# Kernel optimization log

Measured on AMD Instinct MI355X. Metric: run time of the kernel, lower is better.

## Reference

```python
import jax, jax.numpy as jnp
import numpy as np

B, S, D, H = 2, 2048, 1024, 16
DH = D // H
EPS = 1e-5


def _ln(x, g, b):
    m = jnp.mean(x, axis=-1, keepdims=True)
    v = jnp.mean((x - m) ** 2, axis=-1, keepdims=True)
    return (x - m) * jax.lax.rsqrt(v + EPS) * g + b


def setup_inputs() -> dict:
    key = jax.random.key(0)
    ks = jax.random.split(key, 16)
    w = lambda k, shp: jax.random.normal(k, shp, jnp.float32) * 0.02
    return {
        "x": jax.random.normal(ks[0], (B, S, D), jnp.float32),
        # semantic preprocessor: Linear(D,2D) -> ReLU -> Linear(2D,D), residual + LN
        "pW1": w(ks[1], (D, 2 * D)), "pb1": jnp.zeros((2 * D,), jnp.float32),
        "pW2": w(ks[2], (2 * D, D)), "pb2": jnp.zeros((D,), jnp.float32),
        "gp": jnp.ones((D,), jnp.float32), "bp": jnp.zeros((D,), jnp.float32),
        # multi-head attention projections
        "Wq": w(ks[3], (D, D)), "bq": jnp.zeros((D,), jnp.float32),
        "Wk": w(ks[4], (D, D)), "bk": jnp.zeros((D,), jnp.float32),
        "Wv": w(ks[5], (D, D)), "bv": jnp.zeros((D,), jnp.float32),
        "Wo": w(ks[6], (D, D)), "bo": jnp.zeros((D,), jnp.float32),
        "g1": jnp.ones((D,), jnp.float32), "b1": jnp.zeros((D,), jnp.float32),
        # FFN: Linear(D,4D) -> ReLU -> Linear(4D,D)
        "Wf1": w(ks[7], (D, 4 * D)), "bf1": jnp.zeros((4 * D,), jnp.float32),
        "Wf2": w(ks[8], (4 * D, D)), "bf2": jnp.zeros((D,), jnp.float32),
        "g2": jnp.ones((D,), jnp.float32), "b2": jnp.zeros((D,), jnp.float32),
    }


def reference(x, pW1, pb1, pW2, pb2, gp, bp,
              Wq, bq, Wk, bk, Wv, bv, Wo, bo, g1, b1,
              Wf1, bf1, Wf2, bf2, g2, b2):
    # specialized 'semantic' preprocessor (dropout = identity in eval)
    h = jax.nn.relu(x @ pW1 + pb1) @ pW2 + pb2
    s = _ln(x + h, gp, bp)                       # [B,S,D]
    # naive multi-head attention
    q = (s @ Wq + bq).reshape(B, S, H, DH)
    k = (s @ Wk + bk).reshape(B, S, H, DH)
    v = (s @ Wv + bv).reshape(B, S, H, DH)
    scores = jnp.einsum("bqhd,bkhd->bhqk", q, k) / np.sqrt(DH).astype(np.float32)
    attn = jax.nn.softmax(scores, axis=-1)       # [B,H,S,S]
    ctx = jnp.einsum("bhqk,bkhd->bqhd", attn, v).reshape(B, S, D)
    attn_out = ctx @ Wo + bo
    y = _ln(s + attn_out, g1, b1)
    # FFN (dropouts = identity)
    f = jax.nn.relu(y @ Wf1 + bf1) @ Wf2 + bf2
    return _ln(y + f, g2, b2)
```

## Files before the change

### kernel.cpp

```cpp
#include <hip/hip_runtime.h>
#include <cstdint>
#include <cstddef>

typedef _Float16 f16;
typedef _Float16 f16x8 __attribute__((ext_vector_type(8)));
typedef _Float16 f16x4 __attribute__((ext_vector_type(4)));
typedef float    f32x4 __attribute__((ext_vector_type(4)));
typedef float    f32x16 __attribute__((ext_vector_type(16)));
typedef unsigned int uint2v __attribute__((ext_vector_type(2)));

#define MFMA16(a,b,c) __builtin_amdgcn_mfma_f32_16x16x32_f16(a, b, c, 0, 0, 0)
#define MFMA32(a,b,c) __builtin_amdgcn_mfma_f32_32x32x16_f16(a, b, c, 0, 0, 0)

static __device__ __forceinline__ void gload_lds16(const void* g, void* l) {
  __builtin_amdgcn_global_load_lds(
      (const __attribute__((address_space(1))) unsigned int*)g,
      (__attribute__((address_space(3))) unsigned int*)l, 16, 0, 0);
}

static __device__ __forceinline__ int pkh(float a, float b) {
  auto t = __builtin_amdgcn_cvt_pkrtz(a, b);
  return __builtin_bit_cast(int, t);
}

static __device__ __forceinline__ float ex2(float x) {
  return __builtin_amdgcn_exp2f(x);
}

static __device__ __forceinline__ uint2v pswap(int a, int b) {
  return __builtin_amdgcn_permlane32_swap((unsigned)a, (unsigned)b, false, false);
}
static __device__ __forceinline__ float xhalf_max(float x) {
  uint2v r = pswap(__builtin_bit_cast(int, x), __builtin_bit_cast(int, x));
  return fmaxf(__builtin_bit_cast(float, r.x), __builtin_bit_cast(float, r.y));
}
static __device__ __forceinline__ float xhalf_sum(float x) {
  uint2v r = pswap(__builtin_bit_cast(int, x), __builtin_bit_cast(int, x));
  return __builtin_bit_cast(float, r.x) + __builtin_bit_cast(float, r.y);
}

__global__ __launch_bounds__(256) void cast_kernel(const float* __restrict__ x,
                                                   f16* __restrict__ y, int n4) {
  int i = blockIdx.x * 256 + threadIdx.x;
  if (i < n4) {
    float4 v = ((const float4*)x)[i];
    f16x4 h;
    h[0] = (f16)v.x; h[1] = (f16)v.y; h[2] = (f16)v.z; h[3] = (f16)v.w;
    *(f16x4*)(y + (size_t)i * 4) = h;
  }
}

__global__ __launch_bounds__(256) void wtrans(const float* __restrict__ W,
                                              f16* __restrict__ Wt, int K, int N,
                                              float scale) {
  __shared__ float tile[32][33];
  const int n0 = blockIdx.x * 32, k0 = blockIdx.y * 32;
  const int c = threadIdx.x & 31, r = threadIdx.x >> 5;
#pragma unroll
  for (int i = 0; i < 4; i++) {
    int row = r + i * 8;
    tile[row][c] = W[(size_t)(k0 + row) * N + n0 + c];
  }
  __syncthreads();
#pragma unroll
  for (int i = 0; i < 4; i++) {
    int row = r + i * 8;
    Wt[(size_t)(n0 + row) * K + k0 + c] = (f16)(tile[c][row] * scale);
  }
}

__global__ __launch_bounds__(256) void qkvbias_kernel(const float* __restrict__ bq,
                                                      const float* __restrict__ bk,
                                                      const float* __restrict__ bv,
                                                      float* __restrict__ bqkv) {
  int i = blockIdx.x * 256 + threadIdx.x;
  if (i < 1024)       bqkv[i] = bq[i] * 0.18033688f;
  else if (i < 2048)  bqkv[i] = bk[i - 1024];
  else if (i < 3072)  bqkv[i] = bv[i - 2048];
}

template <int MODE, int BN>
__global__ __launch_bounds__(256, 2)
void gemm_kernel(const f16* __restrict__ A, const f16* __restrict__ W,
                 const float* __restrict__ bias, const float* __restrict__ res,
                 void* __restrict__ out, f16* __restrict__ vt, int N, int K) {
  __shared__ __align__(16) f16 lsA[128 * 64];
  __shared__ __align__(16) f16 lsB[BN * 64];
  constexpr int MI = (BN == 128) ? 4 : 2;
  constexpr int NB = (BN == 128) ? 4 : 2;
  const int tid  = threadIdx.x;
  const int lane = tid & 63;
  const int wid  = tid >> 6;
  const int frow = lane & 15;
  const int kgrp = lane >> 4;
  const int wmBase = (BN == 128) ? (wid >> 1) * 64 : wid * 32;
  const int wnBase = (BN == 128) ? (wid & 1) * 64 : 0;
  const int bn = blockIdx.x, bm = blockIdx.y;

  const f32x4 zero4 = {0.f, 0.f, 0.f, 0.f};
  f32x4 acc[MI][4];
#pragma unroll
  for (int i = 0; i < MI; i++)
#pragma unroll
    for (int j = 0; j < 4; j++) acc[i][j] = zero4;

  const f16* aSrc[4]; int lOffA[4];
  const f16* bSrc[NB]; int lOffB[NB];
#pragma unroll
  for (int i = 0; i < 4; i++) {
    int c_lin = i * 256 + wid * 64 + lane;
    int row = c_lin >> 3;
    int ch  = (c_lin & 7) ^ (row & 7);
    aSrc[i] = A + (size_t)(bm * 128 + row) * K + ch * 8;
    lOffA[i] = (i * 256 + wid * 64) * 8;
  }
#pragma unroll
  for (int i = 0; i < NB; i++) {
    int c_lin = i * 256 + wid * 64 + lane;
    int row = c_lin >> 3;
    int ch  = (c_lin & 7) ^ (row & 7);
    bSrc[i] = W + (size_t)(bn * BN + row) * K + ch * 8;
    lOffB[i] = (i * 256 + wid * 64) * 8;
  }

  const int nk = K >> 6;
  for (int ks = 0; ks < nk; ++ks) {
#pragma unroll
    for (int i = 0; i < 4; i++) gload_lds16(aSrc[i] + ks * 64, &lsA[lOffA[i]]);
#pragma unroll
    for (int i = 0; i < NB; i++) gload_lds16(bSrc[i] + ks * 64, &lsB[lOffB[i]]);
    __syncthreads();
#pragma unroll
    for (int kk = 0; kk < 2; kk++) {
      f16x8 af[MI], bf[4];
#pragma unroll
      for (int i = 0; i < MI; i++) {
        int row = wmBase + i * 16 + frow;
        af[i] = *(const f16x8*)&lsA[row * 64 + (((kk * 4 + kgrp) ^ (row & 7)) << 3)];
      }
#pragma unroll
      for (int j = 0; j < 4; j++) {
        int row = wnBase + j * 16 + frow;
        bf[j] = *(const f16x8*)&lsB[row * 64 + (((kk * 4 + kgrp) ^ (row & 7)) << 3)];
      }
#pragma unroll
      for (int i = 0; i < MI; i++)
#pragma unroll
        for (int j = 0; j < 4; j++) acc[i][j] = MFMA16(af[i], bf[j], acc[i][j]);
    }
    __syncthreads();
  }

#pragma unroll
  for (int j = 0; j < 4; j++) {
    const int col = bn * BN + wnBase + j * 16 + frow;
    const float bb = bias[col];
#pragma unroll
    for (int i = 0; i < MI; i++) {
      const int row0 = bm * 128 + wmBase + i * 16 + kgrp * 4;
      if (MODE == 3 && col >= 2048) {
        const int vcol = col - 2048;
        const int bh = (row0 >> 11) * 16 + (vcol >> 6);
        const int d  = vcol & 63;
        const int kv = row0 & 2047;
        f16x4 pk;
#pragma unroll
        for (int r = 0; r < 4; r++) pk[r] = (f16)(acc[i][j][r] + bb);
        *(f16x4*)(vt + ((size_t)bh * 64 + d) * 2048 + kv) = pk;
      } else {
#pragma unroll
        for (int r = 0; r < 4; r++) {
          float v = acc[i][j][r] + bb;
          const size_t idx = (size_t)(row0 + r) * N + col;
          if (MODE == 1) v = fmaxf(v, 0.f);
          if (MODE == 2) ((float*)out)[idx] = v + res[idx];
          else           ((f16*)out)[idx]   = (f16)v;
        }
      }
    }
  }
}

__global__ __launch_bounds__(256, 4)
void attn_kernel(const f16* __restrict__ Qp, const f16* __restrict__ Kp,
                 const f16* __restrict__ Vt, f16* __restrict__ opart,
                 float* __restrict__ Lbuf, int ldq) {
  __shared__ __align__(16) f16 lsKb[2 * 64 * 64];
  __shared__ __align__(16) f16 lsVb[2 * 64 * 64];
  const int tid = threadIdx.x, lane = tid & 63, wid = tid >> 6;
  const int qcol = lane & 31;
  const int hi = lane >> 5;
  const int bid = blockIdx.x;
  const int idx = bid >> 3;
  const int bh = ((bid & 7) << 2) | (idx & 3);
  const int rest = idx >> 2;
  const int part = rest & 1;
  const int qt = rest >> 1;
  const int b = bh >> 4, h = bh & 15;
  const size_t rb = (size_t)b * 2048;
  const int hc = h * 64;
  const int kv0 = part * 1024;
  const int qrow = qt * 128 + wid * 32 + qcol;

  f16x8 qf[4];
  {
    const f16* qp = Qp + (rb + qrow) * ldq + hc;
#pragma unroll
    for (int kc = 0; kc < 4; kc++) qf[kc] = *(const f16x8*)(qp + kc * 16 + hi * 8);
  }

  f32x16 ot0, ot1;
#pragma unroll
  for (int i = 0; i < 16; i++) { ot0[i] = 0.f; ot1[i] = 0.f; }
  float mrun = -1e30f, lrun = 0.f;

  const f16 *kS0, *kS1, *vS0, *vS1;
  int off0, off1;
  {
    int c0 = wid * 64 + lane;
    int r0 = c0 >> 3, ch0 = (c0 & 7) ^ (r0 & 7);
    int c1 = 256 + wid * 64 + lane;
    int r1 = c1 >> 3, ch1 = (c1 & 7) ^ (r1 & 7);
    kS0 = Kp + (rb + kv0 + r0) * ldq + hc + ch0 * 8;
    kS1 = Kp + (rb + kv0 + r1) * ldq + hc + ch1 * 8;
    const f16* vbase = Vt + (size_t)bh * 64 * 2048 + kv0;
    vS0 = vbase + (size_t)r0 * 2048 + ch0 * 8;
    vS1 = vbase + (size_t)r1 * 2048 + ch1 * 8;
    off0 = (wid * 64) * 8;
    off1 = (256 + wid * 64) * 8;
  }

#define ASTAGE(T, PB)                                                    \
  {                                                                      \
    f16* kd = lsKb + (PB) * 4096;                                        \
    f16* vd = lsVb + (PB) * 4096;                                        \
    const size_t ko = (size_t)(T) * 64 * ldq;                            \
    const size_t vo = (size_t)(T) * 64;                                  \
    gload_lds16(kS0 + ko, kd + off0);                                    \
    gload_lds16(kS1 + ko, kd + off1);                                    \
    gload_lds16(vS0 + vo, vd + off0);                                    \
    gload_lds16(vS1 + vo, vd + off1);                                    \
  }

  ASTAGE(0, 0);
  asm volatile("s_waitcnt vmcnt(0)" ::: "memory");
  __builtin_amdgcn_s_barrier();

  for (int kt = 0; kt < 16; ++kt) {
    const int cur = kt & 1;
    if (kt < 15) ASTAGE(kt + 1, cur ^ 1);
    const f16* kb = lsKb + cur * 4096;
    const f16* vb = lsVb + cur * 4096;

    f32x16 s0, s1;
#pragma unroll
    for (int i = 0; i < 16; i++) { s0[i] = 0.f; s1[i] = 0.f; }
    const int kr0 = qcol, kr1 = 32 + qcol;
    __builtin_amdgcn_s_setprio(1);
#pragma unroll
    for (int kc = 0; kc < 4; kc++) {
      f16x8 a0 = *(const f16x8*)&kb[kr0 * 64 + (((kc * 2 + hi) ^ (kr0 & 7)) << 3)];
      f16x8 a1 = *(const f16x8*)&kb[kr1 * 64 + (((kc * 2 + hi) ^ (kr1 & 7)) << 3)];
      s0 = MFMA32(a0, qf[kc], s0);
      s1 = MFMA32(a1, qf[kc], s1);
    }
    __builtin_amdgcn_s_setprio(0);

    float mx[16];
#pragma unroll
    for (int r = 0; r < 16; r++) mx[r] = fmaxf(s0[r], s1[r]);
#pragma unroll
    for (int w = 8; w > 0; w >>= 1)
#pragma unroll
      for (int r = 0; r < w; r++) mx[r] = fmaxf(mx[r], mx[r + w]);
    float pmax = xhalf_max(mx[0]);
    if (__any(pmax > mrun + 11.54f)) {
      float mn = fmaxf(mrun, pmax);
      float fac = ex2(mrun - mn);
      mrun = mn;
      lrun *= fac;
#pragma unroll
      for (int i = 0; i < 16; i++) { ot0[i] *= fac; ot1[i] *= fac; }
    }
#pragma unroll
    for (int r = 0; r < 16; r++) {
      s0[r] = ex2(s0[r] - mrun);
      s1[r] = ex2(s1[r] - mrun);
    }
    float sm[16];
#pragma unroll
    for (int r = 0; r < 16; r++) sm[r] = s0[r] + s1[r];
#pragma unroll
    for (int w = 8; w > 0; w >>= 1)
#pragma unroll
      for (int r = 0; r < w; r++) sm[r] += sm[r + w];
    lrun += xhalf_sum(sm[0]);

#pragma unroll
    for (int st = 0; st < 2; ++st) {
#pragma unroll
      for (int c0 = 0; c0 < 2; c0++) {
        const int c8 = c0 * 8;
        int a0, a1, b0, b1;
        if (st == 0) {
          a0 = pkh(s0[c8 + 0], s0[c8 + 1]); a1 = pkh(s0[c8 + 2], s0[c8 + 3]);
          b0 = pkh(s0[c8 + 4], s0[c8 + 5]); b1 = pkh(s0[c8 + 6], s0[c8 + 7]);
        } else {
          a0 = pkh(s1[c8 + 0], s1[c8 + 1]); a1 = pkh(s1[c8 + 2], s1[c8 + 3]);
          b0 = pkh(s1[c8 + 4], s1[c8 + 5]); b1 = pkh(s1[c8 + 6], s1[c8 + 7]);
        }
        uint2v r0 = pswap(a0, b0);
        uint2v r1 = pswap(a1, b1);
        int4 wv;
        wv.x = (int)r0.x; wv.y = (int)r1.x; wv.z = (int)r0.y; wv.w = (int)r1.y;
        f16x8 pfrag = __builtin_bit_cast(f16x8, wv);
        const int ch = st * 4 + c0 * 2 + hi;
        const int vr0 = qcol, vr1 = 32 + qcol;
        f16x8 av0 = *(const f16x8*)&vb[vr0 * 64 + ((ch ^ (vr0 & 7)) << 3)];
        f16x8 av1 = *(const f16x8*)&vb[vr1 * 64 + ((ch ^ (vr1 & 7)) << 3)];
        __builtin_amdgcn_s_setprio(1);
        ot0 = MFMA32(av0, pfrag, ot0);
        ot1 = MFMA32(av1, pfrag, ot1);
        __builtin_amdgcn_s_setprio(0);
      }
    }
    asm volatile("s_waitcnt vmcnt(0)" ::: "memory");
    __builtin_amdgcn_s_barrier();
  }
#undef ASTAGE

  const float rinv = 1.f / lrun;
  const size_t pbase = ((size_t)part * 32 + bh) * 2048 + qrow;
  f16* pp = opart + pbase * 64;
#pragma unroll
  for (int rr = 0; rr < 16; rr += 2) {
    const int d = (rr & 3) + 8 * (rr >> 2) + 4 * hi;
    *(int*)(pp + d)      = pkh(ot0[rr] * rinv, ot0[rr + 1] * rinv);
    *(int*)(pp + 32 + d) = pkh(ot1[rr] * rinv, ot1[rr + 1] * rinv);
  }
  if (hi == 0) Lbuf[pbase] = mrun + __builtin_amdgcn_logf(lrun);
}

__global__ __launch_bounds__(256)
void combine_kernel(const f16* __restrict__ opart, const float* __restrict__ Lbuf,
                    f16* __restrict__ ctx) {
  const int bid = blockIdx.x;
  const int bh = bid >> 5, qblk = bid & 31;
  const int t = threadIdx.x;
  const int q = qblk * 64 + (t >> 2);
  const int dp = (t & 3) * 16;
  const size_t base = (size_t)bh * 2048 + q;
  const size_t p1o = (size_t)32 * 2048;
  const float L0 = Lbuf[base];
  const float L1 = Lbuf[p1o + base];
  const float L = fmaxf(L0, L1);
  float w0 = ex2(L0 - L), w1 = ex2(L1 - L);
  const float rs = 1.f / (w0 + w1);
  w0 *= rs; w1 *= rs;
  const f16* p0 = opart + base * 64 + dp;
  const f16* p1 = opart + (p1o + base) * 64 + dp;
  f16x8 a0 = *(const f16x8*)p0, a1 = *(const f16x8*)(p0 + 8);
  f16x8 c0 = *(const f16x8*)p1, c1 = *(const f16x8*)(p1 + 8);
  f16x8 o0, o1;
#pragma unroll
  for (int j = 0; j < 8; j++) {
    o0[j] = (f16)(w0 * (float)a0[j] + w1 * (float)c0[j]);
    o1[j] = (f16)(w0 * (float)a1[j] + w1 * (float)c1[j]);
  }
  const int b = bh >> 4, h = bh & 15;
  f16* op = ctx + ((size_t)b * 2048 + q) * 1024 + h * 64 + dp;
  *(f16x8*)op = o0;
  *(f16x8*)(op + 8) = o1;
}

__global__ __launch_bounds__(256)
void ln_kernel(const float* __restrict__ x, const float* __restrict__ g,
               const float* __restrict__ be, float* __restrict__ of,
               f16* __restrict__ ob) {
  const int row = blockIdx.x, t = threadIdx.x;
  const float4 v = ((const float4*)(x + (size_t)row * 1024))[t];
  float s = v.x + v.y + v.z + v.w;
  float q = v.x * v.x + v.y * v.y + v.z * v.z + v.w * v.w;
#pragma unroll
  for (int off = 1; off < 64; off <<= 1) {
    s += __shfl_xor(s, off);
    q += __shfl_xor(q, off);
  }
  __shared__ float ss[4], sq[4];
  if ((t & 63) == 0) { ss[t >> 6] = s; sq[t >> 6] = q; }
  __syncthreads();
  s = ss[0] + ss[1] + ss[2] + ss[3];
  q = sq[0] + sq[1] + sq[2] + sq[3];
  const float mean = s * (1.f / 1024.f);
  const float var  = q * (1.f / 1024.f) - mean * mean;
  const float rstd = rsqrtf(var + 1e-5f);
  const float4 gv = ((const float4*)g)[t];
  const float4 bv = ((const float4*)be)[t];
  float4 ov;
  ov.x = (v.x - mean) * rstd * gv.x + bv.x;
  ov.y = (v.y - mean) * rstd * gv.y + bv.y;
  ov.z = (v.z - mean) * rstd * gv.z + bv.z;
  ov.w = (v.w - mean) * rstd * gv.w + bv.w;
  if (of) ((float4*)(of + (size_t)row * 1024))[t] = ov;
  if (ob) {
    f16x4 hv;
    hv[0] = (f16)ov.x; hv[1] = (f16)ov.y; hv[2] = (f16)ov.z; hv[3] = (f16)ov.w;
    *(f16x4*)(ob + (size_t)row * 1024 + t * 4) = hv;
  }
}

extern "C" void kernel_launch(void* const* d_in, const int* in_sizes, int n_in,
                              void* d_out, int out_size, void* d_ws, size_t ws_size,
                              hipStream_t stream) {
  const float* x   = (const float*)d_in[0];
  const float* pW1 = (const float*)d_in[1];
  const float* pb1 = (const float*)d_in[2];
  const float* pW2 = (const float*)d_in[3];
  const float* pb2 = (const float*)d_in[4];
  const float* gp  = (const float*)d_in[5];
  const float* bp  = (const float*)d_in[6];
  const float* Wq  = (const float*)d_in[7];
  const float* bq  = (const float*)d_in[8];
  const float* Wk  = (const float*)d_in[9];
  const float* bk  = (const float*)d_in[10];
  const float* Wv  = (const float*)d_in[11];
  const float* bv  = (const float*)d_in[12];
  const float* Wo  = (const float*)d_in[13];
  const float* bo  = (const float*)d_in[14];
  const float* g1  = (const float*)d_in[15];
  const float* b1  = (const float*)d_in[16];
  const float* Wf1 = (const float*)d_in[17];
  const float* bf1 = (const float*)d_in[18];
  const float* Wf2 = (const float*)d_in[19];
  const float* bf2 = (const float*)d_in[20];
  const float* g2  = (const float*)d_in[21];
  const float* b2  = (const float*)d_in[22];

  char* ws = (char*)d_ws;
  const size_t MB = 1024 * 1024;
  if (ws_size < 121 * MB) return;

  f16*   wtP1 = (f16*)(ws);
  f16*   wtP2 = (f16*)(ws + 4 * MB);
  f16*   wtQ  = (f16*)(ws + 8 * MB);
  f16*   wtK  = (f16*)(ws + 10 * MB);
  f16*   wtV  = (f16*)(ws + 12 * MB);
  f16*   wtO  = (f16*)(ws + 14 * MB);
  f16*   wtF1 = (f16*)(ws + 16 * MB);
  f16*   wtF2 = (f16*)(ws + 24 * MB);
  f16*   big  = (f16*)(ws + 32 * MB);
  float* t32  = (float*)(ws + 64 * MB);
  float* s32  = (float*)(ws + 80 * MB);
  float* y32  = (float*)(ws + 96 * MB);
  f16*   ybuf = (f16*)(ws + 112 * MB);
  float* bqkv = (float*)(ws + 120 * MB);
  f16* xb    = (f16*)t32;
  f16* sb    = (f16*)y32;
  f16* ctx   = ybuf;
  f16* Vt    = big + (size_t)4096 * 3072;
  f16* opart = (f16*)y32;
  float* Lbuf = t32;

  dim3 blk(256);
  qkvbias_kernel<<<12, blk, 0, stream>>>(bq, bk, bv, bqkv);
  cast_kernel<<<4096, blk, 0, stream>>>(x, xb, 1048576);
  wtrans<<<dim3(64, 32),  blk, 0, stream>>>(pW1, wtP1, 1024, 2048, 1.f);
  wtrans<<<dim3(32, 64),  blk, 0, stream>>>(pW2, wtP2, 2048, 1024, 1.f);
  wtrans<<<dim3(32, 32),  blk, 0, stream>>>(Wq,  wtQ,  1024, 1024, 0.18033688f);
  wtrans<<<dim3(32, 32),  blk, 0, stream>>>(Wk,  wtK,  1024, 1024, 1.f);
  wtrans<<<dim3(32, 32),  blk, 0, stream>>>(Wv,  wtV,  1024, 1024, 1.f);
  wtrans<<<dim3(32, 32),  blk, 0, stream>>>(Wo,  wtO,  1024, 1024, 1.f);
  wtrans<<<dim3(128, 32), blk, 0, stream>>>(Wf1, wtF1, 1024, 4096, 1.f);
  wtrans<<<dim3(32, 128), blk, 0, stream>>>(Wf2, wtF2, 4096, 1024, 1.f);

  gemm_kernel<1,128><<<dim3(16, 32), blk, 0, stream>>>(xb, wtP1, pb1, nullptr, big, nullptr, 2048, 1024);
  gemm_kernel<2,64><<<dim3(16, 32), blk, 0, stream>>>(big, wtP2, pb2, x, t32, nullptr, 1024, 2048);
  ln_kernel<<<4096, blk, 0, stream>>>(t32, gp, bp, s32, sb);
  gemm_kernel<3,128><<<dim3(24, 32), blk, 0, stream>>>(sb, wtQ, bqkv, nullptr, big, Vt, 3072, 1024);
  attn_kernel<<<1024, blk, 0, stream>>>(big, big + 1024, Vt, opart, Lbuf, 3072);
  combine_kernel<<<1024, blk, 0, stream>>>(opart, Lbuf, ctx);
  gemm_kernel<2,64><<<dim3(16, 32), blk, 0, stream>>>(ctx, wtO, bo, s32, t32, nullptr, 1024, 1024);
  ln_kernel<<<4096, blk, 0, stream>>>(t32, g1, b1, y32, ybuf);
  gemm_kernel<1,128><<<dim3(32, 32), blk, 0, stream>>>(ybuf, wtF1, bf1, nullptr, big, nullptr, 4096, 1024);
  gemm_kernel<2,64><<<dim3(16, 32), blk, 0, stream>>>(big, wtF2, bf2, y32, t32, nullptr, 1024, 4096);
  ln_kernel<<<4096, blk, 0, stream>>>(t32, g2, b2, (float*)d_out, nullptr);
}
```

Before: 320.5 us.

## Store residual-stream intermediates in fp16 and remap GEMM blocks per XCD

The residual-add GEMM outputs, LayerNorm inputs and residual sources (x, s, y) now use fp16 buffers instead of fp32, so the memory traffic of the epilogues and LayerNorm kernels is roughly halved. GEMM launches become 1-D grids, with block ids remapped so that each XCD handles a contiguous band of M rows, which is meant to improve L2 reuse of A tiles. The workspace is repacked, with the K and V weights placed contiguously after Q. The fp16 residual path costs precision: x is rounded to fp16 before the first residual add, and LayerNorm statistics come from fp16 sums.

```diff
diff --git a/kernel.cpp b/kernel.cpp
--- a/kernel.cpp
+++ b/kernel.cpp
@@ -82,8 +82,9 @@
 template <int MODE, int BN>
 __global__ __launch_bounds__(256, 2)
 void gemm_kernel(const f16* __restrict__ A, const f16* __restrict__ W,
-                 const float* __restrict__ bias, const float* __restrict__ res,
-                 void* __restrict__ out, f16* __restrict__ vt, int N, int K) {
+                 const float* __restrict__ bias, const f16* __restrict__ res,
+                 void* __restrict__ out, f16* __restrict__ vt, int N, int K,
+                 int gx) {
   __shared__ __align__(16) f16 lsA[128 * 64];
   __shared__ __align__(16) f16 lsB[BN * 64];
   constexpr int MI = (BN == 128) ? 4 : 2;
@@ -95,7 +96,11 @@
   const int kgrp = lane >> 4;
   const int wmBase = (BN == 128) ? (wid >> 1) * 64 : wid * 32;
   const int wnBase = (BN == 128) ? (wid & 1) * 64 : 0;
-  const int bn = blockIdx.x, bm = blockIdx.y;
+
+  const int bid = blockIdx.x;
+  const int xcd = bid & 7, slot = bid >> 3;
+  const int bm = (xcd << 2) + slot / gx;
+  const int bn = slot % gx;
 
   const f32x4 zero4 = {0.f, 0.f, 0.f, 0.f};
   f32x4 acc[MI][4];
@@ -173,8 +178,8 @@
           float v = acc[i][j][r] + bb;
           const size_t idx = (size_t)(row0 + r) * N + col;
           if (MODE == 1) v = fmaxf(v, 0.f);
-          if (MODE == 2) ((float*)out)[idx] = v + res[idx];
-          else           ((f16*)out)[idx]   = (f16)v;
+          if (MODE == 2) v += (float)res[idx];
+          ((f16*)out)[idx] = (f16)v;
         }
       }
     }
@@ -374,13 +379,14 @@
 }
 
 __global__ __launch_bounds__(256)
-void ln_kernel(const float* __restrict__ x, const float* __restrict__ g,
+void ln_kernel(const f16* __restrict__ x, const float* __restrict__ g,
                const float* __restrict__ be, float* __restrict__ of,
                f16* __restrict__ ob) {
   const int row = blockIdx.x, t = threadIdx.x;
-  const float4 v = ((const float4*)(x + (size_t)row * 1024))[t];
-  float s = v.x + v.y + v.z + v.w;
-  float q = v.x * v.x + v.y * v.y + v.z * v.z + v.w * v.w;
+  const f16x4 h4 = *(const f16x4*)(x + (size_t)row * 1024 + t * 4);
+  float v0 = (float)h4[0], v1 = (float)h4[1], v2 = (float)h4[2], v3 = (float)h4[3];
+  float s = v0 + v1 + v2 + v3;
+  float q = v0 * v0 + v1 * v1 + v2 * v2 + v3 * v3;
 #pragma unroll
   for (int off = 1; off < 64; off <<= 1) {
     s += __shfl_xor(s, off);
@@ -397,10 +403,10 @@
   const float4 gv = ((const float4*)g)[t];
   const float4 bv = ((const float4*)be)[t];
   float4 ov;
-  ov.x = (v.x - mean) * rstd * gv.x + bv.x;
-  ov.y = (v.y - mean) * rstd * gv.y + bv.y;
-  ov.z = (v.z - mean) * rstd * gv.z + bv.z;
-  ov.w = (v.w - mean) * rstd * gv.w + bv.w;
+  ov.x = (v0 - mean) * rstd * gv.x + bv.x;
+  ov.y = (v1 - mean) * rstd * gv.y + bv.y;
+  ov.z = (v2 - mean) * rstd * gv.z + bv.z;
+  ov.w = (v3 - mean) * rstd * gv.w + bv.w;
   if (of) ((float4*)(of + (size_t)row * 1024))[t] = ov;
   if (ob) {
     f16x4 hv;
@@ -443,23 +449,21 @@
   f16*   wtP1 = (f16*)(ws);
   f16*   wtP2 = (f16*)(ws + 4 * MB);
   f16*   wtQ  = (f16*)(ws + 8 * MB);
-  f16*   wtK  = (f16*)(ws + 10 * MB);
-  f16*   wtV  = (f16*)(ws + 12 * MB);
   f16*   wtO  = (f16*)(ws + 14 * MB);
   f16*   wtF1 = (f16*)(ws + 16 * MB);
   f16*   wtF2 = (f16*)(ws + 24 * MB);
   f16*   big  = (f16*)(ws + 32 * MB);
-  float* t32  = (float*)(ws + 64 * MB);
-  float* s32  = (float*)(ws + 80 * MB);
-  float* y32  = (float*)(ws + 96 * MB);
-  f16*   ybuf = (f16*)(ws + 112 * MB);
-  float* bqkv = (float*)(ws + 120 * MB);
-  f16* xb    = (f16*)t32;
-  f16* sb    = (f16*)y32;
-  f16* ctx   = ybuf;
-  f16* Vt    = big + (size_t)4096 * 3072;
-  f16* opart = (f16*)y32;
-  float* Lbuf = t32;
+  f16*   xb   = (f16*)(ws + 64 * MB);
+  f16*   tb   = (f16*)(ws + 72 * MB);
+  f16*   sb   = (f16*)(ws + 80 * MB);
+  f16*   ybuf = (f16*)(ws + 88 * MB);
+  f16*   ctx  = (f16*)(ws + 96 * MB);
+  f16*   opart= (f16*)(ws + 104 * MB);
+  float* Lbuf = (float*)(ws + 120 * MB);
+  float* bqkv = (float*)(ws + 120 * MB + 512 * 1024);
+  f16*   wtK  = wtQ + (size_t)1024 * 1024;
+  f16*   wtV  = wtQ + (size_t)2048 * 1024;
+  f16*   Vt   = big + (size_t)4096 * 3072;
 
   dim3 blk(256);
   qkvbias_kernel<<<12, blk, 0, stream>>>(bq, bk, bv, bqkv);
@@ -473,15 +477,15 @@
   wtrans<<<dim3(128, 32), blk, 0, stream>>>(Wf1, wtF1, 1024, 4096, 1.f);
   wtrans<<<dim3(32, 128), blk, 0, stream>>>(Wf2, wtF2, 4096, 1024, 1.f);
 
-  gemm_kernel<1,128><<<dim3(16, 32), blk, 0, stream>>>(xb, wtP1, pb1, nullptr, big, nullptr, 2048, 1024);
-  gemm_kernel<2,64><<<dim3(16, 32), blk, 0, stream>>>(big, wtP2, pb2, x, t32, nullptr, 1024, 2048);
-  ln_kernel<<<4096, blk, 0, stream>>>(t32, gp, bp, s32, sb);
-  gemm_kernel<3,128><<<dim3(24, 32), blk, 0, stream>>>(sb, wtQ, bqkv, nullptr, big, Vt, 3072, 1024);
+  gemm_kernel<1,128><<<512, blk, 0, stream>>>(xb, wtP1, pb1, nullptr, big, nullptr, 2048, 1024, 16);
+  gemm_kernel<2,64><<<512, blk, 0, stream>>>(big, wtP2, pb2, xb, tb, nullptr, 1024, 2048, 16);
+  ln_kernel<<<4096, blk, 0, stream>>>(tb, gp, bp, nullptr, sb);
+  gemm_kernel<3,128><<<768, blk, 0, stream>>>(sb, wtQ, bqkv, nullptr, big, Vt, 3072, 1024, 24);
   attn_kernel<<<1024, blk, 0, stream>>>(big, big + 1024, Vt, opart, Lbuf, 3072);
   combine_kernel<<<1024, blk, 0, stream>>>(opart, Lbuf, ctx);
-  gemm_kernel<2,64><<<dim3(16, 32), blk, 0, stream>>>(ctx, wtO, bo, s32, t32, nullptr, 1024, 1024);
-  ln_kernel<<<4096, blk, 0, stream>>>(t32, g1, b1, y32, ybuf);
-  gemm_kernel<1,128><<<dim3(32, 32), blk, 0, stream>>>(ybuf, wtF1, bf1, nullptr, big, nullptr, 4096, 1024);
-  gemm_kernel<2,64><<<dim3(16, 32), blk, 0, stream>>>(big, wtF2, bf2, y32, t32, nullptr, 1024, 4096);
-  ln_kernel<<<4096, blk, 0, stream>>>(t32, g2, b2, (float*)d_out, nullptr);
-}
+  gemm_kernel<2,64><<<512, blk, 0, stream>>>(ctx, wtO, bo, sb, tb, nullptr, 1024, 1024, 16);
+  ln_kernel<<<4096, blk, 0, stream>>>(tb, g1, b1, nullptr, ybuf);
+  gemm_kernel<1,128><<<1024, blk, 0, stream>>>(ybuf, wtF1, bf1, nullptr, big, nullptr, 4096, 1024, 32);
+  gemm_kernel<2,64><<<512, blk, 0, stream>>>(big, wtF2, bf2, ybuf, tb, nullptr, 1024, 4096, 16);
+  ln_kernel<<<4096, blk, 0, stream>>>(tb, g2, b2, (float*)d_out, nullptr);
+}
```

After: 309.7 us. 3.4% less time.
